# Kernel optimization log

Hardware: AMD Instinct MI355X
Metric: run time of the kernel (lower is better)

Reference implementation:

```python
import jax, jax.numpy as jnp
import numpy as np

THRESHOLD = 0.05
STRIDE = (1, 1)
PADDING = ((1, 1), (1, 1))


def ternary_quantize(w, threshold=THRESHOLD):
    # w -> {-1, 0, +1}; zero where |w| <= threshold
    mask = (jnp.abs(w) > threshold).astype(w.dtype)
    return jnp.sign(w) * mask


def setup_inputs() -> dict:
    key = jax.random.key(0)
    k1, k2 = jax.random.split(key)
    B, Cin, H, W = 32, 256, 56, 56
    Cout, kH, kW = 256, 3, 3
    fan_in = Cin * kH * kW
    std = np.sqrt(2.0 / fan_in) * 2.0
    x = jax.random.normal(k1, (B, Cin, H, W), dtype=jnp.float32)
    weight = jax.random.normal(k2, (Cout, Cin, kH, kW), dtype=jnp.float32) * std
    bias = jnp.zeros((Cout,), dtype=jnp.float32)
    return {"x": x, "weight": weight, "bias": bias}


def reference(x, weight, bias):
    w_t = ternary_quantize(weight, THRESHOLD)
    out = jax.lax.conv_general_dilated(
        x, w_t,
        window_strides=STRIDE,
        padding=PADDING,
        dimension_numbers=("NCHW", "OIHW", "NCHW"),
    )
    return out + bias[None, :, None, None]
```

## Files before the change

### kernel.cpp

```cpp
#include <hip/hip_runtime.h>

#define CIN   256
#define COUT  256
#define HH    56
#define WW    56
#define BATCH 32
#define KTOT  2304
#define HP    58
#define WP    58
#define NPIX  (BATCH*HH*WW)
#define HWSZ  (HH*WW)

typedef __bf16 bf16x8 __attribute__((ext_vector_type(8)));
typedef float  f32x4  __attribute__((ext_vector_type(4)));

#define AS1 __attribute__((address_space(1)))
#define AS3 __attribute__((address_space(3)))

__device__ __forceinline__ unsigned short f2bf(float f) {
  union { float f; unsigned int u; } v; v.f = f;
  unsigned int u = v.u;
  u += 0x7fffu + ((u >> 16) & 1u);
  return (unsigned short)(u >> 16);
}

__device__ __forceinline__ void async16(const void* g, void* l) {
  __builtin_amdgcn_global_load_lds((const AS1 unsigned int*)g,
                                   (AS3 unsigned int*)l, 16, 0, 0);
}

__global__ __launch_bounds__(256) void quant_w(const float* __restrict__ w,
                                               unsigned short* __restrict__ wr) {
  int tid = blockIdx.x * 256 + threadIdx.x;
  if (tid >= COUT * KTOT) return;
  int co  = tid / KTOT;
  int rem = tid - co * KTOT;
  int tap = rem >> 8;
  int ci  = rem & 255;
  int kh  = tap / 3;
  int kw  = tap - kh * 3;
  float v = w[((co * CIN + ci) * 3 + kh) * 3 + kw];
  float q = (fabsf(v) > 0.05f) ? ((v > 0.f) ? 1.f : -1.f) : 0.f;
  wr[tid] = f2bf(q);
}

__global__ __launch_bounds__(256) void pad_nhwc(const float* __restrict__ x,
                                                unsigned short* __restrict__ xp) {
  const int nhp = blockIdx.x;
  const int n   = nhp / HP;
  const int hp  = nhp - n * HP;
  const int ci0 = blockIdx.y * 64;
  const int t   = threadIdx.x;
  const size_t obase = (size_t)nhp * (WP * 256);

  __shared__ __align__(16) float tile[64 * 56];
  const bool hborder = (hp == 0) || (hp == HP - 1);

  if (!hborder) {
    const int h = hp - 1;
    #pragma unroll
    for (int it = 0; it < 4; ++it) {
      int linear = it * 256 + t;
      if (linear < 896) {
        int cil = linear / 14;
        int w4  = linear - cil * 14;
        *(float4*)&tile[cil * 56 + w4 * 4] =
            *(const float4*)&x[(((size_t)(n * CIN + ci0 + cil)) * HH + h) * WW + w4 * 4];
      }
    }
  }
  __syncthreads();

  #pragma unroll
  for (int it = 0; it < 2; ++it) {
    int linear = it * 256 + t;
    if (linear < 464) {
      int wp = linear >> 3;
      int g  = linear & 7;
      unsigned int pk[4] = {0u, 0u, 0u, 0u};
      if (!hborder && wp != 0 && wp != WP - 1) {
        #pragma unroll
        for (int j = 0; j < 4; ++j) {
          unsigned int lo = f2bf(tile[(g * 8 + 2 * j) * 56 + (wp - 1)]);
          unsigned int hi = f2bf(tile[(g * 8 + 2 * j + 1) * 56 + (wp - 1)]);
          pk[j] = lo | (hi << 16);
        }
      }
      uint4 v; v.x = pk[0]; v.y = pk[1]; v.z = pk[2]; v.w = pk[3];
      *(uint4*)(xp + obase + (size_t)wp * 256 + ci0 + g * 8) = v;
    }
  }
}

__global__ __launch_bounds__(256, 2) void conv_gemm(
    const unsigned short* __restrict__ Wr,
    const unsigned short* __restrict__ Xp,
    const float* __restrict__ bias,
    float* __restrict__ out) {
  __shared__ __align__(16) unsigned short a_tile[2][128 * 32];
  __shared__ __align__(16) unsigned short b_tile[2][128 * 32];

  const int t    = threadIdx.x;
  const int lane = t & 63;
  const int wv   = t >> 6;
  const int wm   = wv >> 1;
  const int wn   = wv & 1;
  const int l15  = lane & 15;
  const int quad = lane >> 4;

  const int f   = blockIdx.x;
  const int xcd = f & 7;
  const int pos = f >> 3;
  const int nf  = xcd * 196 + pos;
  const int cob = nf & 1;
  const int pb  = nf >> 1;

  const int co0 = cob * 128;
  const int p0  = pb * 128;

  const int srow = t >> 2;
  const int scol = t & 3;

  const size_t aIdx0 = (size_t)(co0 + srow) * KTOT + scol * 8;
  const size_t aIdx1 = aIdx0 + (size_t)64 * KTOT;

  const int pA = p0 + srow;
  const int pB = pA + 64;
  const int nA = pA / HWSZ;  const int hwA = pA - nA * HWSZ;
  const int hA = hwA / WW;   const int wA  = hwA - hA * WW;
  const int nB = pB / HWSZ;  const int hwB = pB - nB * HWSZ;
  const int hB = hwB / WW;   const int wB  = hwB - hB * WW;
  const size_t bIdx0 = ((size_t)((nA * HP + hA) * WP + wA)) * 256 + scol * 8;
  const size_t bIdx1 = ((size_t)((nB * HP + hB) * WP + wB)) * 256 + scol * 8;

  auto stage = [&](int kk, int s) {
    const int tap   = kk >> 3;
    const int cio   = (kk & 7) << 5;
    const int kh    = tap / 3;
    const int kw    = tap - kh * 3;
    const int koffW = kk << 5;
    const int koffX = (kh * WP + kw) * 256 + cio;
    async16(Wr + koffW + aIdx0, &a_tile[s][0] + t * 8);
    async16(Wr + koffW + aIdx1, &a_tile[s][0] + 2048 + t * 8);
    async16(Xp + koffX + bIdx0, &b_tile[s][0] + t * 8);
    async16(Xp + koffX + bIdx1, &b_tile[s][0] + 2048 + t * 8);
  };

  f32x4 acc[4][4];
  #pragma unroll
  for (int i = 0; i < 4; ++i)
    #pragma unroll
    for (int j = 0; j < 4; ++j)
      acc[i][j] = (f32x4){0.f, 0.f, 0.f, 0.f};

  stage(0, 0);
  __syncthreads();

  for (int kk = 0; kk < KTOT / 32; ++kk) {
    const int cur = kk & 1;
    if (kk < KTOT / 32 - 1)
      stage(kk + 1, cur ^ 1);

    bf16x8 af[4], bfr[4];
    #pragma unroll
    for (int mt = 0; mt < 4; ++mt)
      af[mt] = *(const bf16x8*)(&a_tile[cur][0] +
                                ((wm * 64 + mt * 16 + l15) * 32 + quad * 8));
    #pragma unroll
    for (int nt = 0; nt < 4; ++nt)
      bfr[nt] = *(const bf16x8*)(&b_tile[cur][0] +
                                 ((wn * 64 + nt * 16 + l15) * 32 + quad * 8));

    #pragma unroll
    for (int mt = 0; mt < 4; ++mt)
      #pragma unroll
      for (int nt = 0; nt < 4; ++nt)
        acc[mt][nt] = __builtin_amdgcn_mfma_f32_16x16x32_bf16(
            af[mt], bfr[nt], acc[mt][nt], 0, 0, 0);

    __syncthreads();
  }

  float bv[4][4];
  #pragma unroll
  for (int mt = 0; mt < 4; ++mt)
    #pragma unroll
    for (int r = 0; r < 4; ++r)
      bv[mt][r] = bias[co0 + wm * 64 + mt * 16 + quad * 4 + r];

  #pragma unroll
  for (int nt = 0; nt < 4; ++nt) {
    const int p  = p0 + wn * 64 + nt * 16 + l15;
    const int np = p / HWSZ;
    const int hw = p - np * HWSZ;
    const size_t obase = (size_t)np * (COUT * HWSZ) + hw;
    #pragma unroll
    for (int mt = 0; mt < 4; ++mt) {
      const int co = co0 + wm * 64 + mt * 16 + quad * 4;
      #pragma unroll
      for (int r = 0; r < 4; ++r)
        out[obase + (size_t)(co + r) * HWSZ] = acc[mt][nt][r] + bv[mt][r];
    }
  }
}

extern "C" void kernel_launch(void* const* d_in, const int* in_sizes, int n_in,
                              void* d_out, int out_size, void* d_ws, size_t ws_size,
                              hipStream_t stream) {
  const float* x    = (const float*)d_in[0];
  const float* w    = (const float*)d_in[1];
  const float* bias = (const float*)d_in[2];
  float* out        = (float*)d_out;

  unsigned short* xp = (unsigned short*)d_ws;
  unsigned short* wr = (unsigned short*)((char*)d_ws + 55115776);

  quant_w<<<dim3((COUT * KTOT) / 256), dim3(256), 0, stream>>>(w, wr);
  pad_nhwc<<<dim3(BATCH * HP, 4), dim3(256), 0, stream>>>(x, xp);
  conv_gemm<<<dim3(NPIX / 128 * 2), dim3(256), 0, stream>>>(wr, xp, bias, out);
}
```

Baseline: 337.8 us.

## Rework conv GEMM into 256x256 tiles with swizzled LDS and phased async pipeline

Replaces the 128x128 tile, 256-thread GEMM with 512-thread blocks that each cover all 256 output channels and 256 pixels, using a K-step of 64 split into half-phases. Loads go into 128 KB of dynamic LDS in an XOR-swizzled layout, with a double-buffered pipeline driven by explicit vmcnt waits, raw barriers and setprio around the MFMA bursts. The aim is to raise arithmetic intensity, cut LDS bank conflicts and overlap global loads with compute. In exchange, each CU can hold only one block because of the large LDS footprint, register pressure rises with 32 accumulators per thread, and the grid shrinks to 392 blocks, which may load the CUs unevenly.

```diff
diff --git a/kernel.cpp b/kernel.cpp
--- a/kernel.cpp
+++ b/kernel.cpp
@@ -10,6 +10,7 @@
 #define WP    58
 #define NPIX  (BATCH*HH*WW)
 #define HWSZ  (HH*WW)
+#define KT    36
 
 typedef __bf16 bf16x8 __attribute__((ext_vector_type(8)));
 typedef float  f32x4  __attribute__((ext_vector_type(4)));
@@ -92,101 +93,149 @@
   }
 }
 
-__global__ __launch_bounds__(256, 2) void conv_gemm(
+
+__device__ __forceinline__ int xko_of(int kk) {
+  int tap = kk >> 2;
+  int k3  = tap / 3;
+  int w3  = tap - k3 * 3;
+  return (k3 * WP + w3) * 256 + ((kk & 3) << 6);
+}
+
+#define NOWAIT (void)0
+#define VM8 asm volatile("s_waitcnt vmcnt(8)" ::: "memory")
+#define VM4 asm volatile("s_waitcnt vmcnt(4)" ::: "memory")
+#define VM0 asm volatile("s_waitcnt vmcnt(0)" ::: "memory")
+
+#define STAGE_A(b_, kh_, kkq_) do {                                           \
+  const size_t ko_ = (size_t)(kkq_) * 64 + (kh_) * 32;                        \
+  char* d_ = smem + (((b_) * 2 + (kh_)) * 16384) + t * 16;                    \
+  async16(Wr + aOff0 + ko_, d_);                                              \
+  async16(Wr + aOff1 + ko_, d_ + 8192);                                       \
+} while (0)
+
+#define STAGE_B(b_, kh_, xko_) do {                                           \
+  const size_t ko_ = (size_t)(xko_) + (kh_) * 32;                             \
+  char* d_ = smem + 65536 + (((b_) * 2 + (kh_)) * 16384) + t * 16;            \
+  async16(Xp + bOff0 + ko_, d_);                                              \
+  async16(Xp + bOff1 + ko_, d_ + 8192);                                       \
+} while (0)
+
+#define PHASE(b_, kh_, mh_, WAITE, ...) do {                                  \
+  const int abase_ = ((b_) * 2 + (kh_)) * 16384;                              \
+  const int bbase_ = 65536 + ((b_) * 2 + (kh_)) * 16384;                      \
+  bf16x8 af_[4];                                                              \
+  _Pragma("unroll")                                                           \
+  for (int mt = 0; mt < 4; ++mt)                                              \
+    af_[mt] = *(const bf16x8*)(smem + abase_ + rdA + (mh_) * 4096 + mt * 1024);\
+  if ((mh_) == 0) {                                                           \
+    _Pragma("unroll")                                                         \
+    for (int nt = 0; nt < 4; ++nt)                                            \
+      bfr[nt] = *(const bf16x8*)(smem + bbase_ + rdB + nt * 1024);            \
+  }                                                                           \
+  __VA_ARGS__;                                                                \
+  __builtin_amdgcn_s_barrier();                                               \
+  asm volatile("s_waitcnt lgkmcnt(0)" ::: "memory");                          \
+  __builtin_amdgcn_sched_barrier(0);                                          \
+  __builtin_amdgcn_s_setprio(1);                                              \
+  _Pragma("unroll")                                                           \
+  for (int mt = 0; mt < 4; ++mt)                                              \
+    _Pragma("unroll")                                                         \
+    for (int nt = 0; nt < 4; ++nt)                                            \
+      acc[(mh_) * 4 + mt][nt] = __builtin_amdgcn_mfma_f32_16x16x32_bf16(      \
+          af_[mt], bfr[nt], acc[(mh_) * 4 + mt][nt], 0, 0, 0);                \
+  __builtin_amdgcn_s_setprio(0);                                              \
+  WAITE;                                                                      \
+  __builtin_amdgcn_s_barrier();                                               \
+} while (0)
+
+#define TILE_FULL(b_, kk_) do {                                               \
+  const int kkn1_ = (kk_) + 1, kkn2_ = (kk_) + 2;                             \
+  const int xko1_ = xko_of(kkn1_), xko2_ = xko_of(kkn2_);                     \
+  PHASE(b_, 0, 0, NOWAIT, STAGE_A((b_) ^ 1, 1, kkn1_));                       \
+  PHASE(b_, 0, 1, VM8,    STAGE_B((b_) ^ 1, 1, xko1_));                       \
+  PHASE(b_, 1, 0, NOWAIT, STAGE_A((b_), 0, kkn2_));                           \
+  PHASE(b_, 1, 1, VM8,    STAGE_B((b_), 0, xko2_));                           \
+} while (0)
+
+__global__ __launch_bounds__(512, 2) void conv_gemm(
     const unsigned short* __restrict__ Wr,
     const unsigned short* __restrict__ Xp,
     const float* __restrict__ bias,
     float* __restrict__ out) {
-  __shared__ __align__(16) unsigned short a_tile[2][128 * 32];
-  __shared__ __align__(16) unsigned short b_tile[2][128 * 32];
+  extern __shared__ char smem[];
 
   const int t    = threadIdx.x;
   const int lane = t & 63;
   const int wv   = t >> 6;
-  const int wm   = wv >> 1;
-  const int wn   = wv & 1;
+  const int wm   = wv >> 2;
+  const int wn   = wv & 3;
   const int l15  = lane & 15;
   const int quad = lane >> 4;
 
-  const int f   = blockIdx.x;
-  const int xcd = f & 7;
-  const int pos = f >> 3;
-  const int nf  = xcd * 196 + pos;
-  const int cob = nf & 1;
-  const int pb  = nf >> 1;
-
-  const int co0 = cob * 128;
-  const int p0  = pb * 128;
+  const int bid = blockIdx.x;
+  const int pb  = (bid & 7) * 49 + (bid >> 3);
+  const int p0  = pb * 256;
 
   const int srow = t >> 2;
-  const int scol = t & 3;
-
-  const size_t aIdx0 = (size_t)(co0 + srow) * KTOT + scol * 8;
-  const size_t aIdx1 = aIdx0 + (size_t)64 * KTOT;
+  const int schk = (t & 3) ^ (srow & 3);
+  const size_t aOff0 = (size_t)srow * KTOT + schk * 8;
+  const size_t aOff1 = aOff0 + (size_t)128 * KTOT;
 
   const int pA = p0 + srow;
-  const int pB = pA + 64;
+  const int pB = pA + 128;
   const int nA = pA / HWSZ;  const int hwA = pA - nA * HWSZ;
   const int hA = hwA / WW;   const int wA  = hwA - hA * WW;
   const int nB = pB / HWSZ;  const int hwB = pB - nB * HWSZ;
   const int hB = hwB / WW;   const int wB  = hwB - hB * WW;
-  const size_t bIdx0 = ((size_t)((nA * HP + hA) * WP + wA)) * 256 + scol * 8;
-  const size_t bIdx1 = ((size_t)((nB * HP + hB) * WP + wB)) * 256 + scol * 8;
-
-  auto stage = [&](int kk, int s) {
-    const int tap   = kk >> 3;
-    const int cio   = (kk & 7) << 5;
-    const int kh    = tap / 3;
-    const int kw    = tap - kh * 3;
-    const int koffW = kk << 5;
-    const int koffX = (kh * WP + kw) * 256 + cio;
-    async16(Wr + koffW + aIdx0, &a_tile[s][0] + t * 8);
-    async16(Wr + koffW + aIdx1, &a_tile[s][0] + 2048 + t * 8);
-    async16(Xp + koffX + bIdx0, &b_tile[s][0] + t * 8);
-    async16(Xp + koffX + bIdx1, &b_tile[s][0] + 2048 + t * 8);
-  };
-
-  f32x4 acc[4][4];
-  #pragma unroll
-  for (int i = 0; i < 4; ++i)
+  const size_t bOff0 = ((size_t)((nA * HP + hA) * WP + wA)) * 256 + schk * 8;
+  const size_t bOff1 = ((size_t)((nB * HP + hB) * WP + wB)) * 256 + schk * 8;
+
+  const int rchk = ((quad ^ (l15 & 3)) * 16);
+  const int rdA  = (wm * 128 + l15) * 64 + rchk;
+  const int rdB  = (wn * 64 + l15) * 64 + rchk;
+
+  f32x4 acc[8][4];
+  #pragma unroll
+  for (int i = 0; i < 8; ++i)
     #pragma unroll
     for (int j = 0; j < 4; ++j)
       acc[i][j] = (f32x4){0.f, 0.f, 0.f, 0.f};
-
-  stage(0, 0);
-  __syncthreads();
-
-  for (int kk = 0; kk < KTOT / 32; ++kk) {
-    const int cur = kk & 1;
-    if (kk < KTOT / 32 - 1)
-      stage(kk + 1, cur ^ 1);
-
-    bf16x8 af[4], bfr[4];
-    #pragma unroll
-    for (int mt = 0; mt < 4; ++mt)
-      af[mt] = *(const bf16x8*)(&a_tile[cur][0] +
-                                ((wm * 64 + mt * 16 + l15) * 32 + quad * 8));
-    #pragma unroll
-    for (int nt = 0; nt < 4; ++nt)
-      bfr[nt] = *(const bf16x8*)(&b_tile[cur][0] +
-                                 ((wn * 64 + nt * 16 + l15) * 32 + quad * 8));
-
-    #pragma unroll
-    for (int mt = 0; mt < 4; ++mt)
-      #pragma unroll
-      for (int nt = 0; nt < 4; ++nt)
-        acc[mt][nt] = __builtin_amdgcn_mfma_f32_16x16x32_bf16(
-            af[mt], bfr[nt], acc[mt][nt], 0, 0, 0);
-
-    __syncthreads();
-  }
-
-  float bv[4][4];
-  #pragma unroll
-  for (int mt = 0; mt < 4; ++mt)
+  bf16x8 bfr[4];
+
+  STAGE_A(0, 0, 0);
+  STAGE_B(0, 0, xko_of(0));
+  STAGE_A(0, 1, 0);
+  STAGE_B(0, 1, xko_of(0));
+  STAGE_A(1, 0, 1);
+  STAGE_B(1, 0, xko_of(1));
+  VM8;
+  __builtin_amdgcn_s_barrier();
+
+  #pragma unroll 1
+  for (int kk = 0; kk < 34; kk += 2) {
+    TILE_FULL(0, kk);
+    TILE_FULL(1, kk + 1);
+  }
+  {
+    const int xko35 = xko_of(35);
+    PHASE(0, 0, 0, NOWAIT, STAGE_A(1, 1, 35));
+    PHASE(0, 0, 1, VM8,    STAGE_B(1, 1, xko35));
+    PHASE(0, 1, 0, NOWAIT, NOWAIT);
+    PHASE(0, 1, 1, VM4,    NOWAIT);
+  }
+  {
+    PHASE(1, 0, 0, NOWAIT, NOWAIT);
+    PHASE(1, 0, 1, VM0,    NOWAIT);
+    PHASE(1, 1, 0, NOWAIT, NOWAIT);
+    PHASE(1, 1, 1, NOWAIT, NOWAIT);
+  }
+
+  float bv[8][4];
+  #pragma unroll
+  for (int m = 0; m < 8; ++m)
     #pragma unroll
     for (int r = 0; r < 4; ++r)
-      bv[mt][r] = bias[co0 + wm * 64 + mt * 16 + quad * 4 + r];
+      bv[m][r] = bias[wm * 128 + m * 16 + quad * 4 + r];
 
   #pragma unroll
   for (int nt = 0; nt < 4; ++nt) {
@@ -195,11 +244,11 @@
     const int hw = p - np * HWSZ;
     const size_t obase = (size_t)np * (COUT * HWSZ) + hw;
     #pragma unroll
-    for (int mt = 0; mt < 4; ++mt) {
-      const int co = co0 + wm * 64 + mt * 16 + quad * 4;
+    for (int m = 0; m < 8; ++m) {
+      const int co = wm * 128 + m * 16 + quad * 4;
       #pragma unroll
       for (int r = 0; r < 4; ++r)
-        out[obase + (size_t)(co + r) * HWSZ] = acc[mt][nt][r] + bv[mt][r];
+        out[obase + (size_t)(co + r) * HWSZ] = acc[m][nt][r] + bv[m][r];
     }
   }
 }
@@ -217,5 +266,8 @@
 
   quant_w<<<dim3((COUT * KTOT) / 256), dim3(256), 0, stream>>>(w, wr);
   pad_nhwc<<<dim3(BATCH * HP, 4), dim3(256), 0, stream>>>(x, xp);
-  conv_gemm<<<dim3(NPIX / 128 * 2), dim3(256), 0, stream>>>(wr, xp, bias, out);
-}
+
+  (void)hipFuncSetAttribute((const void*)conv_gemm,
+                            hipFuncAttributeMaxDynamicSharedMemorySize, 131072);
+  conv_gemm<<<dim3(392), dim3(512), 131072, stream>>>(wr, xp, bias, out);
+}
```

After: 342.8 us. About the same (+1.5%).

## Triple-buffer conv GEMM with swizzled LDS, explicit waitcnt and MFMA priority

Applied to the files above, without the earlier changes.

Replaces the double-buffered main loop with a three-stage LDS ring in dynamic shared memory, so two tiles are in flight while one is consumed. The loop uses explicit vmcnt waits, raw barriers and setprio around the MFMA block. LDS chunks are XOR-swizzled to cut bank conflicts on fragment reads, and the pad kernel's tile stride is padded to 60. Occupancy is raised to 3 blocks per CU, which tightens the register budget and relies on hand-written wait counts being correct.

```diff
diff --git a/kernel.cpp b/kernel.cpp
--- a/kernel.cpp
+++ b/kernel.cpp
@@ -44,6 +44,7 @@
   wr[tid] = f2bf(q);
 }
 
+#define TSTR 60
 __global__ __launch_bounds__(256) void pad_nhwc(const float* __restrict__ x,
                                                 unsigned short* __restrict__ xp) {
   const int nhp = blockIdx.x;
@@ -53,7 +54,7 @@
   const int t   = threadIdx.x;
   const size_t obase = (size_t)nhp * (WP * 256);
 
-  __shared__ __align__(16) float tile[64 * 56];
+  __shared__ __align__(16) float tile[64 * TSTR];
   const bool hborder = (hp == 0) || (hp == HP - 1);
 
   if (!hborder) {
@@ -64,7 +65,7 @@
       if (linear < 896) {
         int cil = linear / 14;
         int w4  = linear - cil * 14;
-        *(float4*)&tile[cil * 56 + w4 * 4] =
+        *(float4*)&tile[cil * TSTR + w4 * 4] =
             *(const float4*)&x[(((size_t)(n * CIN + ci0 + cil)) * HH + h) * WW + w4 * 4];
       }
     }
@@ -81,8 +82,8 @@
       if (!hborder && wp != 0 && wp != WP - 1) {
         #pragma unroll
         for (int j = 0; j < 4; ++j) {
-          unsigned int lo = f2bf(tile[(g * 8 + 2 * j) * 56 + (wp - 1)]);
-          unsigned int hi = f2bf(tile[(g * 8 + 2 * j + 1) * 56 + (wp - 1)]);
+          unsigned int lo = f2bf(tile[(g * 8 + 2 * j) * TSTR + (wp - 1)]);
+          unsigned int hi = f2bf(tile[(g * 8 + 2 * j + 1) * TSTR + (wp - 1)]);
           pk[j] = lo | (hi << 16);
         }
       }
@@ -92,13 +93,56 @@
   }
 }
 
-__global__ __launch_bounds__(256, 2) void conv_gemm(
+
+#define NOWAIT (void)0
+#define VM4 asm volatile("s_waitcnt vmcnt(4)" ::: "memory")
+#define VM0 asm volatile("s_waitcnt vmcnt(0)" ::: "memory")
+
+#define STAGE4(buf_, kn_) do {                                                \
+  const int kn__ = (kn_);                                                     \
+  const size_t koW_ = (size_t)kn__ << 5;                                      \
+  const int tap_ = kn__ >> 3;                                                 \
+  const int kh_  = tap_ / 3;                                                  \
+  const int kw_  = tap_ - kh_ * 3;                                            \
+  const size_t koX_ = (size_t)((kh_ * WP + kw_) * 256 + ((kn__ & 7) << 5));   \
+  char* da_ = smem + (buf_) * 8192 + t * 16;                                  \
+  char* db_ = smem + 24576 + (buf_) * 8192 + t * 16;                          \
+  async16(Wr + koW_ + aSrc0, da_);                                            \
+  async16(Wr + koW_ + aSrc1, da_ + 4096);                                     \
+  async16(Xp + koX_ + bSrc0, db_);                                            \
+  async16(Xp + koX_ + bSrc1, db_ + 4096);                                     \
+} while (0)
+
+#define PHASE(buf_, WAITE, ...) do {                                          \
+  __VA_ARGS__;                                                                \
+  bf16x8 af_[4], bf_[4];                                                      \
+  _Pragma("unroll")                                                           \
+  for (int mt = 0; mt < 4; ++mt)                                              \
+    af_[mt] = *(const bf16x8*)(smem + (buf_) * 8192 + rdA + mt * 1024);       \
+  _Pragma("unroll")                                                           \
+  for (int nt = 0; nt < 4; ++nt)                                              \
+    bf_[nt] = *(const bf16x8*)(smem + 24576 + (buf_) * 8192 + rdB + nt * 1024);\
+  __builtin_amdgcn_s_barrier();                                               \
+  asm volatile("s_waitcnt lgkmcnt(0)" ::: "memory");                          \
+  __builtin_amdgcn_sched_barrier(0);                                          \
+  __builtin_amdgcn_s_setprio(1);                                              \
+  _Pragma("unroll")                                                           \
+  for (int mt = 0; mt < 4; ++mt)                                              \
+    _Pragma("unroll")                                                         \
+    for (int nt = 0; nt < 4; ++nt)                                            \
+      acc[mt][nt] = __builtin_amdgcn_mfma_f32_16x16x32_bf16(                  \
+          af_[mt], bf_[nt], acc[mt][nt], 0, 0, 0);                            \
+  __builtin_amdgcn_s_setprio(0);                                              \
+  WAITE;                                                                      \
+  __builtin_amdgcn_s_barrier();                                               \
+} while (0)
+
+__global__ __launch_bounds__(256, 3) void conv_gemm(
     const unsigned short* __restrict__ Wr,
     const unsigned short* __restrict__ Xp,
     const float* __restrict__ bias,
     float* __restrict__ out) {
-  __shared__ __align__(16) unsigned short a_tile[2][128 * 32];
-  __shared__ __align__(16) unsigned short b_tile[2][128 * 32];
+  extern __shared__ char smem[];
 
   const int t    = threadIdx.x;
   const int lane = t & 63;
@@ -108,21 +152,18 @@
   const int l15  = lane & 15;
   const int quad = lane >> 4;
 
-  const int f   = blockIdx.x;
-  const int xcd = f & 7;
-  const int pos = f >> 3;
-  const int nf  = xcd * 196 + pos;
+  const int bid = blockIdx.x;
+  const int nf  = (bid & 7) * 196 + (bid >> 3);
   const int cob = nf & 1;
   const int pb  = nf >> 1;
-
   const int co0 = cob * 128;
   const int p0  = pb * 128;
 
   const int srow = t >> 2;
-  const int scol = t & 3;
-
-  const size_t aIdx0 = (size_t)(co0 + srow) * KTOT + scol * 8;
-  const size_t aIdx1 = aIdx0 + (size_t)64 * KTOT;
+  const int schk = (t & 3) ^ ((srow >> 1) & 3);
+
+  const size_t aSrc0 = (size_t)(co0 + srow) * KTOT + schk * 8;
+  const size_t aSrc1 = aSrc0 + (size_t)64 * KTOT;
 
   const int pA = p0 + srow;
   const int pB = pA + 64;
@@ -130,21 +171,12 @@
   const int hA = hwA / WW;   const int wA  = hwA - hA * WW;
   const int nB = pB / HWSZ;  const int hwB = pB - nB * HWSZ;
   const int hB = hwB / WW;   const int wB  = hwB - hB * WW;
-  const size_t bIdx0 = ((size_t)((nA * HP + hA) * WP + wA)) * 256 + scol * 8;
-  const size_t bIdx1 = ((size_t)((nB * HP + hB) * WP + wB)) * 256 + scol * 8;
-
-  auto stage = [&](int kk, int s) {
-    const int tap   = kk >> 3;
-    const int cio   = (kk & 7) << 5;
-    const int kh    = tap / 3;
-    const int kw    = tap - kh * 3;
-    const int koffW = kk << 5;
-    const int koffX = (kh * WP + kw) * 256 + cio;
-    async16(Wr + koffW + aIdx0, &a_tile[s][0] + t * 8);
-    async16(Wr + koffW + aIdx1, &a_tile[s][0] + 2048 + t * 8);
-    async16(Xp + koffX + bIdx0, &b_tile[s][0] + t * 8);
-    async16(Xp + koffX + bIdx1, &b_tile[s][0] + 2048 + t * 8);
-  };
+  const size_t bSrc0 = ((size_t)((nA * HP + hA) * WP + wA)) * 256 + schk * 8;
+  const size_t bSrc1 = ((size_t)((nB * HP + hB) * WP + wB)) * 256 + schk * 8;
+
+  const int rchk = (quad ^ ((l15 >> 1) & 3)) * 16;
+  const int rdA  = (wm * 64 + l15) * 64 + rchk;
+  const int rdB  = (wn * 64 + l15) * 64 + rchk;
 
   f32x4 acc[4][4];
   #pragma unroll
@@ -153,33 +185,21 @@
     for (int j = 0; j < 4; ++j)
       acc[i][j] = (f32x4){0.f, 0.f, 0.f, 0.f};
 
-  stage(0, 0);
-  __syncthreads();
-
-  for (int kk = 0; kk < KTOT / 32; ++kk) {
-    const int cur = kk & 1;
-    if (kk < KTOT / 32 - 1)
-      stage(kk + 1, cur ^ 1);
-
-    bf16x8 af[4], bfr[4];
-    #pragma unroll
-    for (int mt = 0; mt < 4; ++mt)
-      af[mt] = *(const bf16x8*)(&a_tile[cur][0] +
-                                ((wm * 64 + mt * 16 + l15) * 32 + quad * 8));
-    #pragma unroll
-    for (int nt = 0; nt < 4; ++nt)
-      bfr[nt] = *(const bf16x8*)(&b_tile[cur][0] +
-                                 ((wn * 64 + nt * 16 + l15) * 32 + quad * 8));
-
-    #pragma unroll
-    for (int mt = 0; mt < 4; ++mt)
-      #pragma unroll
-      for (int nt = 0; nt < 4; ++nt)
-        acc[mt][nt] = __builtin_amdgcn_mfma_f32_16x16x32_bf16(
-            af[mt], bfr[nt], acc[mt][nt], 0, 0, 0);
-
-    __syncthreads();
-  }
+  STAGE4(0, 0);
+  STAGE4(1, 1);
+  VM4;
+  __builtin_amdgcn_s_barrier();
+
+  #pragma unroll 1
+  for (int it = 0; it < 23; ++it) {
+    const int k0 = 3 * it;
+    PHASE(0, VM4, STAGE4(2, k0 + 2));
+    PHASE(1, VM4, STAGE4(0, k0 + 3));
+    PHASE(2, VM4, STAGE4(1, k0 + 4));
+  }
+  PHASE(0, VM4, STAGE4(2, 71));
+  PHASE(1, VM0, NOWAIT);
+  PHASE(2, NOWAIT, NOWAIT);
 
   float bv[4][4];
   #pragma unroll
@@ -217,5 +237,8 @@
 
   quant_w<<<dim3((COUT * KTOT) / 256), dim3(256), 0, stream>>>(w, wr);
   pad_nhwc<<<dim3(BATCH * HP, 4), dim3(256), 0, stream>>>(x, xp);
-  conv_gemm<<<dim3(NPIX / 128 * 2), dim3(256), 0, stream>>>(wr, xp, bias, out);
-}
+
+  (void)hipFuncSetAttribute((const void*)conv_gemm,
+                            hipFuncAttributeMaxDynamicSharedMemorySize, 49152);
+  conv_gemm<<<dim3(1568), dim3(256), 49152, stream>>>(wr, xp, bias, out);
+}
```

Result: no change. 331.9 us (-1.7%).
